# Kernel tuning notes

Measured on AMD Instinct MI355X. Metric: run time of the kernel, lower is better.

Reference implementation:

```python
import jax, jax.numpy as jnp
import numpy as np

K = 16  # K_neighbors

def linear_positions(pixels):
    # normalized flat (pixels, 2) grid positions, matching LinearPositions(normalize=True, flat_output=True)
    wd = int(round(pixels ** 0.5))
    h = jnp.repeat(jnp.arange(wd, dtype=jnp.float32)[:, None], wd, axis=1)
    w = jnp.repeat(jnp.arange(wd, dtype=jnp.float32)[None, :], wd, axis=0)
    pos = jnp.stack([h, w], axis=-1) / (wd - 1)
    return pos.reshape(pixels, 2)


def setup_inputs() -> dict:
    key = jax.random.key(0)
    ks = jax.random.split(key, 8)
    B, Wn, P, C = 4, 16, 256, 32
    inp = {
        "x": jax.random.normal(ks[0], (B, Wn, P, C), dtype=jnp.float32),
        "sf_w0": jax.random.normal(ks[1], (3 * K, 128), dtype=jnp.float32) * 0.05,
        "sf_b0": jnp.zeros((128,), jnp.float32),
        "sf_w1": jax.random.normal(ks[2], (128, 128), dtype=jnp.float32) * 0.05,
        "sf_b1": jnp.zeros((128,), jnp.float32),
        "sf_wo": jax.random.normal(ks[3], (128, 64), dtype=jnp.float32) * 0.05,
        "sf_bo": jnp.zeros((64,), jnp.float32),
        "out_w0": jax.random.normal(ks[4], (C + 64, 128), dtype=jnp.float32) * 0.05,
        "out_b0": jnp.zeros((128,), jnp.float32),
        "out_w1": jax.random.normal(ks[5], (128, 128), dtype=jnp.float32) * 0.05,
        "out_b1": jnp.zeros((128,), jnp.float32),
        "out_wo": jax.random.normal(ks[6], (128, 64), dtype=jnp.float32) * 0.05,
        "out_bo": jnp.zeros((64,), jnp.float32),
    }
    return inp


def reference(x, sf_w0, sf_b0, sf_w1, sf_b1, sf_wo, sf_bo,
              out_w0, out_b0, out_w1, out_b1, out_wo, out_bo):
    B, Wn, P, C = x.shape
    # L1 similarity: 1 - mean |x_i - x_j| over channels -> (B, Wn, P, P)
    w = 1.0 - jnp.mean(jnp.abs(x[:, :, :, None, :] - x[:, :, None, :, :]), axis=-1)
    K_scores, K_idxs = jax.lax.top_k(w, K)  # (B, Wn, P, K)
    pos = linear_positions(P)  # (P, 2)
    # source pos for pixel i minus gathered target pos of its K neighbors
    rel = pos[None, None, :, None, :] - pos[K_idxs]  # (B, Wn, P, K, 2)
    K_rel_pos = rel.reshape(B, Wn, P, K * 2)
    # sf FFN
    h = jnp.concatenate([K_scores, K_rel_pos], axis=-1)  # (B, Wn, P, 3K)
    h = jax.nn.relu(h @ sf_w0 + sf_b0)
    h = jax.nn.relu(h @ sf_w1 + sf_b1)
    sf = h @ sf_wo + sf_bo  # (B, Wn, P, 64)
    # out FFN
    h = jnp.concatenate([x, sf], axis=-1)  # (B, Wn, P, C+64)
    h = jax.nn.relu(h @ out_w0 + out_b0)
    h = jax.nn.relu(h @ out_w1 + out_b1)
    return h @ out_wo + out_bo  # (B, Wn, P, 64)
```

## Files before the change

kernel.cpp:

```cpp
#include <hip/hip_runtime.h>
#include <hip/hip_bf16.h>

#define K_SEL 16
#define NCAND 20

typedef __attribute__((ext_vector_type(8))) short short8;
typedef __attribute__((ext_vector_type(4))) short short4v;
typedef __attribute__((ext_vector_type(4))) float f32x4;

__device__ __forceinline__ short f2bf_bits(float v) {
    union { __hip_bfloat16 b; short s; } u;
    u.b = __float2bfloat16(v);
    return u.s;
}
__device__ __forceinline__ float bf2f_bits(short h) {
    return __uint_as_float(((unsigned)(unsigned short)h) << 16);
}
__device__ __forceinline__ float readlane_f(float v, int l) {
    return __int_as_float(__builtin_amdgcn_readlane(__float_as_int(v), l));
}

template<int COMP>
__device__ __forceinline__ void simtopk_body(
    const float* __restrict__ x, float* __restrict__ feat,
    float* xsT, int* candj, double* rs, int win, int grp, int tid)
{
    const int lane = tid & 63;
    const int wv   = tid >> 6;

    if (tid < 512) {
        const int c4 = tid & 7, jb = tid >> 3;
        const float4* gx = reinterpret_cast<const float4*>(x + (size_t)win * 8192);
        float4 v0 = gx[jb * 8 + c4];
        float4 v1 = gx[jb * 8 + c4 + 512];
        float4 v2 = gx[jb * 8 + c4 + 1024];
        float4 v3 = gx[jb * 8 + c4 + 1536];
        float4* xsT4 = reinterpret_cast<float4*>(xsT);
        const int gsw = jb ^ c4;
        xsT4[(4 * c4 + 0) * 64 + gsw] = make_float4(v0.x, v1.x, v2.x, v3.x);
        xsT4[(4 * c4 + 1) * 64 + gsw] = make_float4(v0.y, v1.y, v2.y, v3.y);
        xsT4[(4 * c4 + 2) * 64 + gsw] = make_float4(v0.z, v1.z, v2.z, v3.z);
        xsT4[(4 * c4 + 3) * 64 + gsw] = make_float4(v0.w, v1.w, v2.w, v3.w);
    }
    __syncthreads();

    const int plbase = (grp & 1) * 32 + wv * 2;

    const f32x4* xsT4c = reinterpret_cast<const f32x4*>(xsT);
    float acc0[4] = {0.f, 0.f, 0.f, 0.f};
    float acc1[4] = {0.f, 0.f, 0.f, 0.f};
    #pragma unroll
    for (int c = 0; c < 32; ++c) {
        f32x4 a = xsT4c[c * 64 + (lane ^ ((c >> 2) & 7))];
        float xi0 = readlane_f(a[COMP], plbase);
        float xi1 = readlane_f(a[COMP], plbase + 1);
        #pragma unroll
        for (int q = 0; q < 4; ++q) {
            acc0[q] += fabsf(a[q] - xi0);
            acc1[q] += fabsf(a[q] - xi1);
        }
    }
    unsigned int p0[4], p1[4];
    #pragma unroll
    for (int q = 0; q < 4; ++q) {
        p0[q] = (__float_as_uint(acc0[q]) & 0xFFFFFF00u) | (unsigned)(q * 64 + lane);
        p1[q] = (__float_as_uint(acc1[q]) & 0xFFFFFF00u) | (unsigned)(q * 64 + lane);
    }

    unsigned int T0 = 0, T1 = 0;
    for (int bit = 31; bit >= 0; --bit) {
        unsigned int c0 = T0 | (1u << bit), c1 = T1 | (1u << bit);
        int n0 = __popcll(__ballot(p0[0] < c0)) + __popcll(__ballot(p0[1] < c0))
               + __popcll(__ballot(p0[2] < c0)) + __popcll(__ballot(p0[3] < c0));
        int n1 = __popcll(__ballot(p1[0] < c1)) + __popcll(__ballot(p1[1] < c1))
               + __popcll(__ballot(p1[2] < c1)) + __popcll(__ballot(p1[3] < c1));
        if (n0 < NCAND) T0 = c0;
        if (n1 < NCAND) T1 = c1;
    }

    const unsigned long long lt = (1ull << lane) - 1ull;
    int base0 = 0, base1 = 0;
    #pragma unroll
    for (int q = 0; q < 4; ++q) {
        bool s0 = (p0[q] <= T0);
        unsigned long long m0 = __ballot(s0);
        if (s0) candj[(wv * 2 + 0) * NCAND + base0 + __popcll(m0 & lt)] = q * 64 + lane;
        base0 += __popcll(m0);
        bool s1 = (p1[q] <= T1);
        unsigned long long m1 = __ballot(s1);
        if (s1) candj[(wv * 2 + 1) * NCAND + base1 + __popcll(m1 & lt)] = q * 64 + lane;
        base1 += __popcll(m1);
    }
    asm volatile("s_waitcnt lgkmcnt(0)" ::: "memory");

    const int t  = lane >> 5;
    const int cl = lane & 31;
    double s = 0.0;
    int myj = -1;
    if (cl < NCAND) {
        myj = candj[(wv * 2 + t) * NCAND + cl];
        const int jl = myj & 63, jq = myj >> 6;
        const int pl = plbase + t;
        #pragma unroll
        for (int c = 0; c < 32; ++c) {
            float xiv = xsT[(c * 64 + (pl ^ ((c >> 2) & 7))) * 4 + COMP];
            float bv  = xsT[(c * 64 + (jl ^ ((c >> 2) & 7))) * 4 + jq];
            s += fabs((double)xiv - (double)bv);
        }
        rs[(wv * 2 + t) * NCAND + cl] = s;
    }
    asm volatile("s_waitcnt lgkmcnt(0)" ::: "memory");

    if (cl < NCAND) {
        int rank = 0;
        #pragma unroll 4
        for (int o = 0; o < NCAND; ++o) {
            double so = rs[(wv * 2 + t) * NCAND + o];
            int    jo = candj[(wv * 2 + t) * NCAND + o];
            rank += (so < s || (so == s && jo < myj)) ? 1 : 0;
        }
        if (rank < K_SEL) {
            const int pwin = grp * 32 + wv * 2 + t;
            const int gp   = win * 256 + pwin;
            feat[gp * 48 + rank] = (float)(1.0 - s * 0.03125);
            float dh = (float)((pwin >> 4) - (myj >> 4)) * (1.0f / 15.0f);
            float dw = (float)((pwin & 15) - (myj & 15)) * (1.0f / 15.0f);
            reinterpret_cast<float2*>(feat)[gp * 24 + 8 + rank] = make_float2(dh, dw);
        }
    }
}

__global__ __launch_bounds__(1024) void simtopk_kernel(
    const float* __restrict__ x,
    float* __restrict__ feat)
{
    __shared__ __align__(16) float xsT[8192];
    __shared__ int    candj[16 * 2 * NCAND];
    __shared__ double rs[16 * 2 * NCAND];

    const int tid = threadIdx.x;
    const int win = blockIdx.x >> 3;
    const int grp = blockIdx.x & 7;

    switch (grp >> 1) {
        case 0: simtopk_body<0>(x, feat, xsT, candj, rs, win, grp, tid); break;
        case 1: simtopk_body<1>(x, feat, xsT, candj, rs, win, grp, tid); break;
        case 2: simtopk_body<2>(x, feat, xsT, candj, rs, win, grp, tid); break;
        default: simtopk_body<3>(x, feat, xsT, candj, rs, win, grp, tid); break;
    }
}

__global__ __launch_bounds__(256) void pack_kernel(
    const float* __restrict__ s0w, const float* __restrict__ s1w,
    const float* __restrict__ sow, const float* __restrict__ o0w,
    const float* __restrict__ o1w, const float* __restrict__ oow,
    short* __restrict__ wpack)
{
    int t = blockIdx.x * 256 + threadIdx.x;
    if (t >= 69632) return;
    int l, base;
    if      (t <  8192) { l = 0; base = 0;     }
    else if (t < 24576) { l = 1; base = 8192;  }
    else if (t < 32768) { l = 2; base = 24576; }
    else if (t < 45056) { l = 3; base = 32768; }
    else if (t < 61440) { l = 4; base = 45056; }
    else                { l = 5; base = 61440; }

    const float* W = (l == 0) ? s0w : (l == 1) ? s1w : (l == 2) ? sow
                   : (l == 3) ? o0w : (l == 4) ? o1w : oow;
    int N    = (l == 2 || l == 5) ? 64 : 128;
    int Kr   = (l == 0) ? 48 : (l == 3) ? 96 : 128;
    int woff = (l == 0) ? 0 : (l == 1) ? 16384 : (l == 2) ? 49152
             : (l == 3) ? 65536 : (l == 4) ? 90112 : 122880;
    int sz   = (l == 2 || l == 5) ? 8192 : (l == 3) ? 12288 : (l == 0) ? 8192 : 16384;

    int e = t - base;
    int i = e & 7, kb = (e >> 3) & 3, rem = e >> 5;
    int n = rem % N, ks = rem / N;
    int k = ks * 32 + kb * 8 + i;
    float v = (k < Kr) ? W[k * N + n] : 0.0f;
    short hi = f2bf_bits(v);
    float lo = v - bf2f_bits(hi);
    wpack[woff + e]      = hi;
    wpack[woff + sz + e] = f2bf_bits(lo);
}

template<int K_STEPS, int N, bool RELU, bool TO_GLOBAL>
__device__ __forceinline__ void bf16_layer(
    const short* hiIn, const short* loIn, short* hiOut, short* loOut,
    float* gout, int pbase, const short* __restrict__ wpack, int woff, int sz,
    const float* __restrict__ bias, int wv, int lane, int out_col_off)
{
    if (N == 64 && wv >= 8) return;
    const int mt  = wv & 1;
    const int nt  = wv >> 1;
    const int m_a = mt * 16 + (lane & 15);
    const int kb  = lane >> 4;
    const int n   = nt * 16 + (lane & 15);

    f32x4 acc = (f32x4){0.f, 0.f, 0.f, 0.f};
    #pragma unroll
    for (int ks = 0; ks < K_STEPS; ++ks) {
        const int g   = ks * 4 + kb;
        const int off = m_a * 256 + ((g ^ (m_a & 7)) << 4);
        short8 ahi = *(const short8*)((const char*)hiIn + off);
        short8 alo = *(const short8*)((const char*)loIn + off);
        const int wi = woff + ((ks * N + n) * 4 + kb) * 8;
        short8 whi = *(const short8*)(wpack + wi);
        short8 wlo = *(const short8*)(wpack + wi + sz);
        acc = __builtin_amdgcn_mfma_f32_16x16x32_bf16(ahi, whi, acc, 0, 0, 0);
        acc = __builtin_amdgcn_mfma_f32_16x16x32_bf16(ahi, wlo, acc, 0, 0, 0);
        acc = __builtin_amdgcn_mfma_f32_16x16x32_bf16(alo, whi, acc, 0, 0, 0);
    }

    const float bv = bias[n];
    #pragma unroll
    for (int r = 0; r < 4; ++r) {
        float v = acc[r] + bv;
        if (RELU) v = fmaxf(v, 0.0f);
        const int pw = mt * 16 + (lane >> 4) * 4 + r;
        if (TO_GLOBAL) {
            gout[(size_t)(pbase + pw) * 64 + n] = v;
        } else {
            const int w   = out_col_off + n;
            const int off = pw * 256 + ((((w >> 3) ^ (pw & 7))) << 4) + (w & 7) * 2;
            short h = f2bf_bits(v);
            short l = f2bf_bits(v - bf2f_bits(h));
            *(short*)((char*)hiOut + off) = h;
            *(short*)((char*)loOut + off) = l;
        }
    }
}

__global__ __launch_bounds__(1024) void ffn_kernel(
    const float* __restrict__ x,
    const float* __restrict__ feat,
    const short* __restrict__ wpack,
    const float* __restrict__ s0b, const float* __restrict__ s1b,
    const float* __restrict__ sob, const float* __restrict__ o0b,
    const float* __restrict__ o1b, const float* __restrict__ oob,
    float* __restrict__ out)
{
    __shared__ __align__(16) short hiA[32 * 128];
    __shared__ __align__(16) short loA[32 * 128];
    __shared__ __align__(16) short hiB[32 * 128];
    __shared__ __align__(16) short loB[32 * 128];

    const int tid   = threadIdx.x;
    const int lane  = tid & 63;
    const int wv    = tid >> 6;
    const int pbase = blockIdx.x * 32;

    if (tid < 384) {
        int p = tid / 12, c4 = tid - p * 12;
        f32x4 v = ((const f32x4*)feat)[(size_t)(pbase + p) * 12 + c4];
        short4v h4, l4;
        #pragma unroll
        for (int j = 0; j < 4; ++j) {
            short h = f2bf_bits(v[j]);
            h4[j] = h;
            l4[j] = f2bf_bits(v[j] - bf2f_bits(h));
        }
        int off = p * 256 + ((((c4 >> 1) ^ (p & 7))) << 4) + (c4 & 1) * 8;
        *(short4v*)((char*)hiA + off) = h4;
        *(short4v*)((char*)loA + off) = l4;
    } else if (tid < 512) {
        int t2 = tid - 384;
        int p = t2 & 31, sel = t2 >> 5;
        int g = 6 + (sel & 1);
        int off = p * 256 + ((g ^ (p & 7)) << 4);
        short8 z = (short8){0,0,0,0,0,0,0,0};
        if (sel >> 1) *(short8*)((char*)loA + off) = z;
        else          *(short8*)((char*)hiA + off) = z;
    }
    __syncthreads();

    bf16_layer<2, 128, true, false>(hiA, loA, hiB, loB, nullptr, pbase,
                                    wpack, 0, 8192, s0b, wv, lane, 0);
    __syncthreads();
    bf16_layer<4, 128, true, false>(hiB, loB, hiA, loA, nullptr, pbase,
                                    wpack, 16384, 16384, s1b, wv, lane, 0);
    __syncthreads();
    if (tid < 256) {
        int p = tid >> 3, c4 = tid & 7;
        f32x4 v = ((const f32x4*)x)[(size_t)(pbase + p) * 8 + c4];
        short4v h4, l4;
        #pragma unroll
        for (int j = 0; j < 4; ++j) {
            short h = f2bf_bits(v[j]);
            h4[j] = h;
            l4[j] = f2bf_bits(v[j] - bf2f_bits(h));
        }
        int off = p * 256 + ((((c4 >> 1) ^ (p & 7))) << 4) + (c4 & 1) * 8;
        *(short4v*)((char*)hiB + off) = h4;
        *(short4v*)((char*)loB + off) = l4;
    }
    bf16_layer<4, 64, false, false>(hiA, loA, hiB, loB, nullptr, pbase,
                                    wpack, 49152, 8192, sob, wv, lane, 32);
    __syncthreads();
    bf16_layer<3, 128, true, false>(hiB, loB, hiA, loA, nullptr, pbase,
                                    wpack, 65536, 12288, o0b, wv, lane, 0);
    __syncthreads();
    bf16_layer<4, 128, true, false>(hiA, loA, hiB, loB, nullptr, pbase,
                                    wpack, 90112, 16384, o1b, wv, lane, 0);
    __syncthreads();
    bf16_layer<4, 64, false, true>(hiB, loB, nullptr, nullptr, out, pbase,
                                   wpack, 122880, 8192, oob, wv, lane, 0);
}

extern "C" void kernel_launch(void* const* d_in, const int* in_sizes, int n_in,
                              void* d_out, int out_size, void* d_ws, size_t ws_size,
                              hipStream_t stream) {
    const float* x    = (const float*)d_in[0];
    const float* s0w  = (const float*)d_in[1];
    const float* s0b  = (const float*)d_in[2];
    const float* s1w  = (const float*)d_in[3];
    const float* s1b  = (const float*)d_in[4];
    const float* sow  = (const float*)d_in[5];
    const float* sob  = (const float*)d_in[6];
    const float* o0w  = (const float*)d_in[7];
    const float* o0b  = (const float*)d_in[8];
    const float* o1w  = (const float*)d_in[9];
    const float* o1b  = (const float*)d_in[10];
    const float* oow  = (const float*)d_in[11];
    const float* oob  = (const float*)d_in[12];

    short* wpack = (short*)d_ws;
    float* feat  = (float*)((char*)d_ws + 524288);
    float* out   = (float*)d_out;

    pack_kernel<<<272, 256, 0, stream>>>(s0w, s1w, sow, o0w, o1w, oow, wpack);
    simtopk_kernel<<<512, 1024, 0, stream>>>(x, feat);
    ffn_kernel<<<512, 1024, 0, stream>>>(x, feat, wpack,
                                         s0b, s1b, sob, o0b, o1b, oob,
                                         out);
}
```

Before: 52.98 us.

## Fuse weight packing into similarity kernel and rescore candidates from global memory

Drops the separate pack kernel launch: 68 extra blocks of the simtopk grid now do the weight packing, so pack and similarity work run in one launch. Candidate rescoring in double precision now reads the source and neighbor rows as float4 from global memory instead of strided transposed shared-memory reads. This also recomputes the pixel index from COMP and plbase. It saves one launch and some LDS traffic, at the cost of extra global (mostly L2-cached) loads and possible register pressure from the noinline pack path.

```diff
diff --git a/kernel.cpp b/kernel.cpp
--- a/kernel.cpp
+++ b/kernel.cpp
@@ -18,6 +18,41 @@
 }
 __device__ __forceinline__ float readlane_f(float v, int l) {
     return __int_as_float(__builtin_amdgcn_readlane(__float_as_int(v), l));
+}
+
+__device__ __noinline__ void pack_body(
+    int t,
+    const float* __restrict__ s0w, const float* __restrict__ s1w,
+    const float* __restrict__ sow, const float* __restrict__ o0w,
+    const float* __restrict__ o1w, const float* __restrict__ oow,
+    short* __restrict__ wpack)
+{
+    if (t >= 69632) return;
+    int l, base;
+    if      (t <  8192) { l = 0; base = 0;     }
+    else if (t < 24576) { l = 1; base = 8192;  }
+    else if (t < 32768) { l = 2; base = 24576; }
+    else if (t < 45056) { l = 3; base = 32768; }
+    else if (t < 61440) { l = 4; base = 45056; }
+    else                { l = 5; base = 61440; }
+
+    const float* W = (l == 0) ? s0w : (l == 1) ? s1w : (l == 2) ? sow
+                   : (l == 3) ? o0w : (l == 4) ? o1w : oow;
+    int N    = (l == 2 || l == 5) ? 64 : 128;
+    int Kr   = (l == 0) ? 48 : (l == 3) ? 96 : 128;
+    int woff = (l == 0) ? 0 : (l == 1) ? 16384 : (l == 2) ? 49152
+             : (l == 3) ? 65536 : (l == 4) ? 90112 : 122880;
+    int sz   = (l == 2 || l == 5) ? 8192 : (l == 3) ? 12288 : (l == 0) ? 8192 : 16384;
+
+    int e = t - base;
+    int i = e & 7, kb = (e >> 3) & 3, rem = e >> 5;
+    int n = rem % N, ks = rem / N;
+    int k = ks * 32 + kb * 8 + i;
+    float v = (k < Kr) ? W[k * N + n] : 0.0f;
+    short hi = f2bf_bits(v);
+    float lo = v - bf2f_bits(hi);
+    wpack[woff + e]      = hi;
+    wpack[woff + sz + e] = f2bf_bits(lo);
 }
 
 template<int COMP>
@@ -99,13 +134,17 @@
     int myj = -1;
     if (cl < NCAND) {
         myj = candj[(wv * 2 + t) * NCAND + cl];
-        const int jl = myj & 63, jq = myj >> 6;
-        const int pl = plbase + t;
+        const int pwin = COMP * 64 + plbase + t;
+        const float4* xj = reinterpret_cast<const float4*>(x + (size_t)win * 8192 + (size_t)myj * 32);
+        const float4* xp = reinterpret_cast<const float4*>(x + (size_t)win * 8192 + (size_t)pwin * 32);
         #pragma unroll
-        for (int c = 0; c < 32; ++c) {
-            float xiv = xsT[(c * 64 + (pl ^ ((c >> 2) & 7))) * 4 + COMP];
-            float bv  = xsT[(c * 64 + (jl ^ ((c >> 2) & 7))) * 4 + jq];
-            s += fabs((double)xiv - (double)bv);
+        for (int c4 = 0; c4 < 8; ++c4) {
+            float4 b = xj[c4];
+            float4 a = xp[c4];
+            s += fabs((double)a.x - (double)b.x);
+            s += fabs((double)a.y - (double)b.y);
+            s += fabs((double)a.z - (double)b.z);
+            s += fabs((double)a.w - (double)b.w);
         }
         rs[(wv * 2 + t) * NCAND + cl] = s;
     }
@@ -120,7 +159,7 @@
             rank += (so < s || (so == s && jo < myj)) ? 1 : 0;
         }
         if (rank < K_SEL) {
-            const int pwin = grp * 32 + wv * 2 + t;
+            const int pwin = COMP * 64 + plbase + t;
             const int gp   = win * 256 + pwin;
             feat[gp * 48 + rank] = (float)(1.0 - s * 0.03125);
             float dh = (float)((pwin >> 4) - (myj >> 4)) * (1.0f / 15.0f);
@@ -132,13 +171,24 @@
 
 __global__ __launch_bounds__(1024) void simtopk_kernel(
     const float* __restrict__ x,
-    float* __restrict__ feat)
+    float* __restrict__ feat,
+    const float* __restrict__ s0w, const float* __restrict__ s1w,
+    const float* __restrict__ sow, const float* __restrict__ o0w,
+    const float* __restrict__ o1w, const float* __restrict__ oow,
+    short* __restrict__ wpack)
 {
     __shared__ __align__(16) float xsT[8192];
     __shared__ int    candj[16 * 2 * NCAND];
     __shared__ double rs[16 * 2 * NCAND];
 
     const int tid = threadIdx.x;
+
+    if (blockIdx.x >= 512) {
+        pack_body((blockIdx.x - 512) * 1024 + tid,
+                  s0w, s1w, sow, o0w, o1w, oow, wpack);
+        return;
+    }
+
     const int win = blockIdx.x >> 3;
     const int grp = blockIdx.x & 7;
 
@@ -148,41 +198,6 @@
         case 2: simtopk_body<2>(x, feat, xsT, candj, rs, win, grp, tid); break;
         default: simtopk_body<3>(x, feat, xsT, candj, rs, win, grp, tid); break;
     }
-}
-
-__global__ __launch_bounds__(256) void pack_kernel(
-    const float* __restrict__ s0w, const float* __restrict__ s1w,
-    const float* __restrict__ sow, const float* __restrict__ o0w,
-    const float* __restrict__ o1w, const float* __restrict__ oow,
-    short* __restrict__ wpack)
-{
-    int t = blockIdx.x * 256 + threadIdx.x;
-    if (t >= 69632) return;
-    int l, base;
-    if      (t <  8192) { l = 0; base = 0;     }
-    else if (t < 24576) { l = 1; base = 8192;  }
-    else if (t < 32768) { l = 2; base = 24576; }
-    else if (t < 45056) { l = 3; base = 32768; }
-    else if (t < 61440) { l = 4; base = 45056; }
-    else                { l = 5; base = 61440; }
-
-    const float* W = (l == 0) ? s0w : (l == 1) ? s1w : (l == 2) ? sow
-                   : (l == 3) ? o0w : (l == 4) ? o1w : oow;
-    int N    = (l == 2 || l == 5) ? 64 : 128;
-    int Kr   = (l == 0) ? 48 : (l == 3) ? 96 : 128;
-    int woff = (l == 0) ? 0 : (l == 1) ? 16384 : (l == 2) ? 49152
-             : (l == 3) ? 65536 : (l == 4) ? 90112 : 122880;
-    int sz   = (l == 2 || l == 5) ? 8192 : (l == 3) ? 12288 : (l == 0) ? 8192 : 16384;
-
-    int e = t - base;
-    int i = e & 7, kb = (e >> 3) & 3, rem = e >> 5;
-    int n = rem % N, ks = rem / N;
-    int k = ks * 32 + kb * 8 + i;
-    float v = (k < Kr) ? W[k * N + n] : 0.0f;
-    short hi = f2bf_bits(v);
-    float lo = v - bf2f_bits(hi);
-    wpack[woff + e]      = hi;
-    wpack[woff + sz + e] = f2bf_bits(lo);
 }
 
 template<int K_STEPS, int N, bool RELU, bool TO_GLOBAL>
@@ -329,8 +344,8 @@
     float* feat  = (float*)((char*)d_ws + 524288);
     float* out   = (float*)d_out;
 
-    pack_kernel<<<272, 256, 0, stream>>>(s0w, s1w, sow, o0w, o1w, oow, wpack);
-    simtopk_kernel<<<512, 1024, 0, stream>>>(x, feat);
+    simtopk_kernel<<<580, 1024, 0, stream>>>(x, feat,
+                                             s0w, s1w, sow, o0w, o1w, oow, wpack);
     ffn_kernel<<<512, 1024, 0, stream>>>(x, feat, wpack,
                                          s0b, s1b, sob, o0b, o1b, oob,
                                          out);
```

New measurement: 53.73 us. No clear change (+1.4%).
